# Performance work log

Measured on AMD Instinct MI355X. Metric: run time of the kernel, lower is better.

## Reference

```python
import jax, jax.numpy as jnp
import numpy as np
import math

L = 4      # model_layers
D = 512    # model_filters
H = 32     # heads = max(D//16, 1)
DH = D // H  # 16
S = 1024   # dataset_dimension == max_len == seq_len
B = 2
EPS = 1e-5


def setup_inputs() -> dict:
    key = jax.random.key(0)
    ks = jax.random.split(key, 12)
    scale = 0.02
    n = lambda k, shape: jax.random.normal(k, shape, dtype=jnp.float32) * scale
    return {
        "x": jax.random.normal(ks[0], (B, S), dtype=jnp.float32),
        "Winit": n(ks[1], (D,)),               # init_linear weight (1->D)
        "binit": jnp.zeros((D,), jnp.float32),
        "Wq": n(ks[2], (L, D, D)), "bq": jnp.zeros((L, D), jnp.float32),
        "Wk": n(ks[3], (L, D, D)), "bk": jnp.zeros((L, D), jnp.float32),
        "Wv": n(ks[4], (L, D, D)), "bv": jnp.zeros((L, D), jnp.float32),
        "Er": jax.random.normal(ks[5], (L, S, DH), dtype=jnp.float32) * scale,
        "Wlin": n(ks[6], (L, D, D)), "blin": jnp.zeros((L, D), jnp.float32),
        "ln_g": jnp.ones((L, D), jnp.float32), "ln_b": jnp.zeros((L, D), jnp.float32),
        "Wout": n(ks[7], (D, 1)),              # output_linear, no bias
    }


def layernorm(x, g, b):
    mu = jnp.mean(x, axis=-1, keepdims=True)
    var = jnp.mean(jnp.square(x - mu), axis=-1, keepdims=True)
    return (x - mu) * jax.lax.rsqrt(var + EPS) * g + b


def rel_attn(h, Wq, bq, Wk, bk, Wv, bv, Er):
    # h: [B, S, D]
    b_, s_, _ = h.shape
    q = (h @ Wq + bq).reshape(b_, s_, H, DH).transpose(0, 2, 1, 3)  # [B,H,S,dh]
    k = (h @ Wk + bk).reshape(b_, s_, H, DH).transpose(0, 2, 1, 3)
    v = (h @ Wv + bv).reshape(b_, s_, H, DH).transpose(0, 2, 1, 3)
    # relative-position term with skew trick (seq_len == max_len -> full Er)
    QEr = jnp.einsum('bhsd,td->bhst', q, Er)                  # [B,H,S,S]
    padded = jnp.pad(QEr, ((0, 0), (0, 0), (0, 0), (1, 0)))   # pad left of last dim
    Srel = padded.reshape(b_, H, s_ + 1, s_)[:, :, 1:, :]     # skew
    scores = (jnp.einsum('bhsd,bhtd->bhst', q, k) + Srel) / math.sqrt(DH)
    mask = jnp.tril(jnp.ones((s_, s_), dtype=bool))           # causal
    scores = jnp.where(mask, scores, -jnp.inf)
    p = jax.nn.softmax(scores, axis=-1)
    o = jnp.einsum('bhst,bhtd->bhsd', p, v)
    return o.transpose(0, 2, 1, 3).reshape(b_, s_, D)


def reference(x, Winit, binit, Wq, bq, Wk, bk, Wv, bv, Er, Wlin, blin, ln_g, ln_b, Wout):
    # init_linear(1->D) on scalar per position, then exact gelu
    h = jax.nn.gelu(x[..., None] * Winit + binit, approximate=False)  # [B,S,D]
    for l in range(L):
        a = rel_attn(h, Wq[l], bq[l], Wk[l], bk[l], Wv[l], bv[l], Er[l])
        y = layernorm(a @ Wlin[l] + blin[l], ln_g[l], ln_b[l])
        h = h + jax.nn.gelu(y, approximate=False)
    return h.sum(axis=-2) @ Wout  # [B,1]
```

## Files before the change

kernel.cpp:

```cpp
#include <hip/hip_runtime.h>
#include <math.h>

#define NL 4
#define DIM 512
#define NH 32
#define DHD 16
#define SEQ 1024
#define NB 2
#define LN_EPS 1e-5f
#define NEGF (-1e30f)
#define QSC 0.36067376022224085f

typedef _Float16 half4 __attribute__((ext_vector_type(4)));
typedef _Float16 half8 __attribute__((ext_vector_type(8)));
typedef float floatx4 __attribute__((ext_vector_type(4)));

__device__ __forceinline__ float gelu_exact(float x) {
    return 0.5f * x * (1.0f + erff(x * 0.70710678118654752f));
}

__device__ __forceinline__ void async16(const void* g, void* l) {
    __builtin_amdgcn_global_load_lds(
        (const __attribute__((address_space(1))) void*)g,
        (__attribute__((address_space(3))) void*)l, 16, 0, 0);
}

__global__ __launch_bounds__(256) void k_prep_all(const float* __restrict__ Wq,
        const float* __restrict__ Wk, const float* __restrict__ Wv,
        const float* __restrict__ Wlin, const float* __restrict__ bq,
        const float* __restrict__ bk, const float* __restrict__ bv,
        const float* __restrict__ Er, const float* __restrict__ x,
        const float* __restrict__ Wi, const float* __restrict__ bi,
        _Float16* __restrict__ Wqkvt, _Float16* __restrict__ Wlint,
        float* __restrict__ bqkv, _Float16* __restrict__ Erh,
        float* __restrict__ h, _Float16* __restrict__ hf) {
    __shared__ _Float16 lt[64][72];
    const int u = blockIdx.x;
    const int tid = threadIdx.x;
    if (u < 1024) {
        const int kx = u & 7, ny = (u >> 3) & 7, mz = u >> 6;
        const int l = mz >> 2, which = mz & 3;
        const float* src = (which == 0) ? Wq : (which == 1) ? Wk : (which == 2) ? Wv : Wlin;
        src += (size_t)l * 262144;
        const float scale = (which == 0) ? QSC : 1.0f;
        _Float16* dst = (which < 3) ? (Wqkvt + (size_t)l * 786432 + (size_t)which * 262144)
                                    : (Wlint + (size_t)l * 262144);
        const int k0 = kx << 6, n0 = ny << 6;
        #pragma unroll
        for (int p = 0; p < 4; p++) {
            int kl = (p << 4) + (tid >> 4);
            int n4 = (tid & 15) << 2;
            float4 wv = *(const float4*)(src + (size_t)(k0 + kl) * 512 + n0 + n4);
            lt[n4 + 0][kl] = (_Float16)(wv.x * scale);
            lt[n4 + 1][kl] = (_Float16)(wv.y * scale);
            lt[n4 + 2][kl] = (_Float16)(wv.z * scale);
            lt[n4 + 3][kl] = (_Float16)(wv.w * scale);
        }
        __syncthreads();
        int nl = tid >> 2, k16 = (tid & 3) << 4;
        float4* d4 = (float4*)(dst + (size_t)(n0 + nl) * 512 + k0 + k16);
        const float4* s4 = (const float4*)&lt[nl][k16];
        d4[0] = s4[0];
        d4[1] = s4[1];
    } else if (u < 2048) {
        int idx0 = ((u - 1024) << 10) + (tid << 2);
        int d = idx0 & 511, bs = idx0 >> 9;
        float xs = x[bs];
        float4 wv = *(const float4*)(Wi + d);
        float4 bv = *(const float4*)(bi + d);
        float4 r;
        r.x = gelu_exact(xs * wv.x + bv.x);
        r.y = gelu_exact(xs * wv.y + bv.y);
        r.z = gelu_exact(xs * wv.z + bv.z);
        r.w = gelu_exact(xs * wv.w + bv.w);
        *(float4*)(h + idx0) = r;
        half4 rh = {(_Float16)r.x, (_Float16)r.y, (_Float16)r.z, (_Float16)r.w};
        *(half4*)(hf + idx0) = rh;
    } else {
        int idx = ((u - 2048) << 8) + tid;
        if (idx < NL * 1536) {
            int l = idx / 1536, j = idx % 1536;
            int which = j >> 9, jj = j & 511;
            float val = (which == 0) ? bq[l * 512 + jj] * QSC
                      : (which == 1) ? bk[l * 512 + jj] : bv[l * 512 + jj];
            bqkv[idx] = val;
        }
        int e = idx - NL * 1536;
        if (e >= 0 && e < NL * SEQ * DHD) Erh[e] = (_Float16)Er[e];
    }
}

__global__ __launch_bounds__(256) void k_gemm_qkv(const _Float16* __restrict__ A,
        const _Float16* __restrict__ Bt, const float* __restrict__ bias,
        _Float16* __restrict__ o16) {
    __shared__ _Float16 As[2][128][32];
    __shared__ _Float16 Bs[2][96][32];
    const int tid = threadIdx.x;
    const int w = tid >> 6, lane = tid & 63;
    const int nn = lane & 15, qd = lane >> 4;
    const int wm = (w & 1) << 6;
    const int wn = (w >> 1) * 48;
    const int m0 = blockIdx.x << 7;
    const int n0 = blockIdx.y * 96;
    const int srow = lane >> 2, scol = (lane & 3) << 3;
    floatx4 acc[4][3] = {};
    for (int k0 = 0; k0 < 512; k0 += 64) {
        __syncthreads();
        #pragma unroll
        for (int p = 0; p < 2; p++) {
            #pragma unroll
            for (int hh = 0; hh < 2; hh++)
                async16(A + (size_t)(m0 + (hh << 6) + (w << 4) + srow) * 512
                          + k0 + (p << 5) + scol,
                        &As[p][(hh << 6) + (w << 4)][0]);
            async16(Bt + (size_t)(n0 + (w << 4) + srow) * 512 + k0 + (p << 5) + scol,
                    &Bs[p][(w << 4)][0]);
            if (w < 2)
                async16(Bt + (size_t)(n0 + 64 + (w << 4) + srow) * 512
                           + k0 + (p << 5) + scol,
                        &Bs[p][64 + (w << 4)][0]);
        }
        __syncthreads();
        #pragma unroll
        for (int ks = 0; ks < 2; ks++) {
            half8 af[4], bf[3];
            #pragma unroll
            for (int t = 0; t < 4; t++)
                af[t] = *(const half8*)&As[ks][wm + (t << 4) + nn][qd << 3];
            #pragma unroll
            for (int t = 0; t < 3; t++)
                bf[t] = *(const half8*)&Bs[ks][wn + (t << 4) + nn][qd << 3];
            #pragma unroll
            for (int ti = 0; ti < 4; ti++)
                #pragma unroll
                for (int tj = 0; tj < 3; tj++)
                    acc[ti][tj] = __builtin_amdgcn_mfma_f32_16x16x32_f16(
                            af[ti], bf[tj], acc[ti][tj], 0, 0, 0);
        }
    }
    float bv3[3];
    #pragma unroll
    for (int tj = 0; tj < 3; tj++) bv3[tj] = bias[n0 + wn + (tj << 4) + nn];
    #pragma unroll
    for (int ti = 0; ti < 4; ti++) {
        int rg = m0 + wm + (ti << 4) + (qd << 2);
        #pragma unroll
        for (int tj = 0; tj < 3; tj++) {
            int colg = n0 + wn + (tj << 4) + nn;
            int which = colg >> 9, ci = colg & 511;
            _Float16* op = o16 + (size_t)which * 1048576 + (size_t)rg * 512 + ci;
            #pragma unroll
            for (int r = 0; r < 4; r++)
                op[(size_t)r * 512] = (_Float16)(acc[ti][tj][r] + bv3[tj]);
        }
    }
}

__global__ __launch_bounds__(256) void k_gemm_lin(const _Float16* __restrict__ A,
        const _Float16* __restrict__ Bt, const float* __restrict__ bias,
        float* __restrict__ y) {
    __shared__ _Float16 As[2 * 64 * 32];
    __shared__ _Float16 Bs[2 * 64 * 32];
    const int tid = threadIdx.x;
    const int w = tid >> 6, lane = tid & 63;
    const int nn = lane & 15, qd = lane >> 4;
    const int wm = (w & 1) << 5, wn = (w >> 1) << 5;
    const int m0 = blockIdx.x << 6, n0 = blockIdx.y << 6;
    const int l2r = lane >> 2, l2c = (lane & 3) << 3;
    const _Float16* Ag = A + (size_t)(m0 + (w << 4) + l2r) * 512 + l2c;
    const _Float16* Bg = Bt + (size_t)(n0 + (w << 4) + l2r) * 512 + l2c;
    _Float16* Al = As + (w << 9);
    _Float16* Bl = Bs + (w << 9);
    floatx4 acc[2][2] = {};
    for (int k0 = 0; k0 < 512; k0 += 64) {
        __syncthreads();
        #pragma unroll
        for (int p = 0; p < 2; p++) {
            async16(Ag + k0 + (p << 5), Al + (p << 11));
            async16(Bg + k0 + (p << 5), Bl + (p << 11));
        }
        __syncthreads();
        #pragma unroll
        for (int ks = 0; ks < 2; ks++) {
            half8 af[2], bf[2];
            #pragma unroll
            for (int t = 0; t < 2; t++) {
                af[t] = *(const half8*)&As[(ks << 11) + ((wm + (t << 4) + nn) << 5) + (qd << 3)];
                bf[t] = *(const half8*)&Bs[(ks << 11) + ((wn + (t << 4) + nn) << 5) + (qd << 3)];
            }
            #pragma unroll
            for (int ti = 0; ti < 2; ti++)
                #pragma unroll
                for (int tj = 0; tj < 2; tj++)
                    acc[ti][tj] = __builtin_amdgcn_mfma_f32_16x16x32_f16(
                            af[ti], bf[tj], acc[ti][tj], 0, 0, 0);
        }
    }
    float bv2[2];
    #pragma unroll
    for (int tj = 0; tj < 2; tj++) bv2[tj] = bias[n0 + wn + (tj << 4) + nn];
    #pragma unroll
    for (int ti = 0; ti < 2; ti++) {
        int rg = m0 + wm + (ti << 4) + (qd << 2);
        #pragma unroll
        for (int tj = 0; tj < 2; tj++) {
            int colg = n0 + wn + (tj << 4) + nn;
            float* op = y + (size_t)rg * 512 + colg;
            #pragma unroll
            for (int r = 0; r < 4; r++)
                op[(size_t)r * 512] = acc[ti][tj][r] + bv2[tj];
        }
    }
}

__global__ __launch_bounds__(512) void k_attn_mfma(const _Float16* __restrict__ q,
        const _Float16* __restrict__ k, const _Float16* __restrict__ v,
        const _Float16* __restrict__ Er, _Float16* __restrict__ aout) {
    __shared__ _Float16 Ks[256][20];
    __shared__ _Float16 Vts[16][268];
    __shared__ float Rel[8][16][84];
    const int tid = threadIdx.x;
    const int w = tid >> 6, lane = tid & 63;
    const int wg = w & 3, half = w >> 2;
    const int nn = lane & 15, a4 = (lane >> 4) << 2;
    const int b_ = blockIdx.x >> 5, h_ = blockIdx.x & 31;
    const int y = blockIdx.y;
    const int r0p[2] = {64 * y, 64 * (15 - y)};
    const int R = r0p[1] + 64;

    half4 qf[2];
    floatx4 O[2];
    float m[2], lsum[2];
    #pragma unroll
    for (int ph = 0; ph < 2; ph++) {
        int s0w = r0p[ph] + (wg << 4);
        qf[ph] = *(const half4*)(q + ((size_t)(b_ * SEQ + s0w + nn)) * DIM + h_ * DHD + a4);
        O[ph] = (floatx4){0.f, 0.f, 0.f, 0.f};
        m[ph] = NEGF;
        lsum[ph] = 0.f;
    }

    for (int part = 0; part < 4; part++) {
        const int p0 = part << 8;
        if (p0 >= R) break;
        const int pend = (R < p0 + 256) ? R : (p0 + 256);
        __syncthreads();
        {
            int rl0 = tid >> 2, c4 = (tid & 3) << 2;
            for (int g = 0; g < pend - p0; g += 128) {
                int rl = g + rl0;
                if (rl < pend - p0) {
                    size_t gb = ((size_t)(b_ * SEQ + p0 + rl)) * DIM + h_ * DHD + c4;
                    *(half4*)&Ks[rl][c4] = *(const half4*)(k + gb);
                    half4 vv4 = *(const half4*)(v + gb);
                    Vts[c4 + 0][rl] = vv4.x;
                    Vts[c4 + 1][rl] = vv4.y;
                    Vts[c4 + 2][rl] = vv4.z;
                    Vts[c4 + 3][rl] = vv4.w;
                }
            }
        }
        __syncthreads();
        #pragma unroll
        for (int ph = 0; ph < 2; ph++) {
            const int r0 = r0p[ph];
            const int s0w = r0 + (wg << 4);
            const int hi = (r0 + 64 < pend) ? (r0 + 64) : pend;
            for (int ct = p0; ct < hi; ct += 64) {
                if (((ct >> 6) & 1) != half) continue;
                const int ctl = ct - p0;
                const int jbw = 1008 - s0w + ct;
                #pragma unroll
                for (int jt = 0; jt < 5; jt++) {
                    int j = jbw + (jt << 4) + nn;
                    j = (j < SEQ - 1) ? j : (SEQ - 1);
                    half4 ef = *(const half4*)(Er + (size_t)j * DHD + a4);
                    floatx4 racc = {0.f, 0.f, 0.f, 0.f};
                    racc = __builtin_amdgcn_mfma_f32_16x16x16f16(ef, qf[ph], racc, 0, 0, 0);
                    *(floatx4*)&Rel[w][nn][(jt << 4) + a4] = racc;
                }
                float st[4][4];
                const bool diag = (ct == r0);
                #pragma unroll
                for (int tt = 0; tt < 4; tt++) {
                    half4 kf = *(const half4*)&Ks[ctl + (tt << 4) + nn][a4];
                    floatx4 sacc = {0.f, 0.f, 0.f, 0.f};
                    sacc = __builtin_amdgcn_mfma_f32_16x16x16f16(kf, qf[ph], sacc, 0, 0, 0);
                    const float* rp = &Rel[w][nn][15 - nn + (tt << 4) + a4];
                    #pragma unroll
                    for (int r = 0; r < 4; r++) {
                        int tl = (tt << 4) + a4 + r;
                        float sv = sacc[r] + rp[r];
                        if (diag && (tl > (wg << 4) + nn)) sv = NEGF;
                        st[tt][r] = sv;
                    }
                }
                float cmax = NEGF;
                #pragma unroll
                for (int tt = 0; tt < 4; tt++)
                    #pragma unroll
                    for (int r = 0; r < 4; r++) cmax = fmaxf(cmax, st[tt][r]);
                cmax = fmaxf(cmax, __shfl_xor(cmax, 16));
                cmax = fmaxf(cmax, __shfl_xor(cmax, 32));
                float mnew = fmaxf(m[ph], cmax);
                float alpha = exp2f(m[ph] - mnew);
                m[ph] = mnew;
                float csum = 0.f;
                half4 pf[4];
                #pragma unroll
                for (int tt = 0; tt < 4; tt++) {
                    float p0e = exp2f(st[tt][0] - mnew);
                    float p1e = exp2f(st[tt][1] - mnew);
                    float p2e = exp2f(st[tt][2] - mnew);
                    float p3e = exp2f(st[tt][3] - mnew);
                    csum += (p0e + p1e) + (p2e + p3e);
                    half4 ph4 = {(_Float16)p0e, (_Float16)p1e, (_Float16)p2e, (_Float16)p3e};
                    pf[tt] = ph4;
                }
                lsum[ph] = lsum[ph] * alpha + csum;
                O[ph][0] *= alpha; O[ph][1] *= alpha; O[ph][2] *= alpha; O[ph][3] *= alpha;
                #pragma unroll
                for (int tt = 0; tt < 4; tt++) {
                    half4 vf = *(const half4*)&Vts[nn][ctl + (tt << 4) + a4];
                    O[ph] = __builtin_amdgcn_mfma_f32_16x16x16f16(vf, pf[tt], O[ph], 0, 0, 0);
                }
            }
        }
    }
    float* mb = (float*)Rel;
    __syncthreads();
    if (half == 1) {
        #pragma unroll
        for (int ph = 0; ph < 2; ph++) {
            int base = (((wg << 1) + ph) << 6) + lane;
            mb[base]        = O[ph][0];
            mb[base + 1024] = O[ph][1];
            mb[base + 2048] = O[ph][2];
            mb[base + 3072] = O[ph][3];
            mb[base + 4096] = m[ph];
            mb[base + 5120] = lsum[ph];
        }
    }
    __syncthreads();
    if (half == 0) {
        #pragma unroll
        for (int ph = 0; ph < 2; ph++) {
            int base = (((wg << 1) + ph) << 6) + lane;
            float m1 = mb[base + 4096];
            float l1 = mb[base + 5120];
            float mm = fmaxf(m[ph], m1);
            float a0 = exp2f(m[ph] - mm);
            float a1 = exp2f(m1 - mm);
            float lt = lsum[ph] * a0 + l1 * a1;
            lt += __shfl_xor(lt, 16);
            lt += __shfl_xor(lt, 32);
            float linv = 1.0f / lt;
            float o0 = (O[ph][0] * a0 + mb[base]        * a1) * linv;
            float o1 = (O[ph][1] * a0 + mb[base + 1024] * a1) * linv;
            float o2 = (O[ph][2] * a0 + mb[base + 2048] * a1) * linv;
            float o3 = (O[ph][3] * a0 + mb[base + 3072] * a1) * linv;
            int s0w = r0p[ph] + (wg << 4);
            half4 ov = {(_Float16)o0, (_Float16)o1, (_Float16)o2, (_Float16)o3};
            *(half4*)(aout + ((size_t)(b_ * SEQ + s0w + nn)) * DIM + h_ * DHD + a4) = ov;
        }
    }
}

__global__ __launch_bounds__(256) void k_ln_gelu_res(const float* __restrict__ y,
        const float* __restrict__ gam, const float* __restrict__ bet,
        float* __restrict__ h, _Float16* __restrict__ hf) {
    int row = (blockIdx.x << 2) + (threadIdx.x >> 6);
    int lane = threadIdx.x & 63;
    const float* yr = y + (size_t)row * DIM + (lane << 3);
    float4 v0 = *(const float4*)(yr);
    float4 v1 = *(const float4*)(yr + 4);
    float sum = (v0.x + v0.y) + (v0.z + v0.w) + (v1.x + v1.y) + (v1.z + v1.w);
    float sq = v0.x*v0.x + v0.y*v0.y + v0.z*v0.z + v0.w*v0.w
             + v1.x*v1.x + v1.y*v1.y + v1.z*v1.z + v1.w*v1.w;
    #pragma unroll
    for (int off = 32; off > 0; off >>= 1) {
        sum += __shfl_xor(sum, off);
        sq  += __shfl_xor(sq, off);
    }
    float mu = sum * (1.0f / DIM);
    float var = sq * (1.0f / DIM) - mu * mu;
    float rs = rsqrtf(var + LN_EPS);
    float4 g0 = *(const float4*)(gam + (lane << 3));
    float4 g1 = *(const float4*)(gam + (lane << 3) + 4);
    float4 b0 = *(const float4*)(bet + (lane << 3));
    float4 b1 = *(const float4*)(bet + (lane << 3) + 4);
    float* hr = h + (size_t)row * DIM + (lane << 3);
    float4 h0 = *(const float4*)(hr);
    float4 h1 = *(const float4*)(hr + 4);
    float o[8];
    o[0] = h0.x + gelu_exact((v0.x - mu) * rs * g0.x + b0.x);
    o[1] = h0.y + gelu_exact((v0.y - mu) * rs * g0.y + b0.y);
    o[2] = h0.z + gelu_exact((v0.z - mu) * rs * g0.z + b0.z);
    o[3] = h0.w + gelu_exact((v0.w - mu) * rs * g0.w + b0.w);
    o[4] = h1.x + gelu_exact((v1.x - mu) * rs * g1.x + b1.x);
    o[5] = h1.y + gelu_exact((v1.y - mu) * rs * g1.y + b1.y);
    o[6] = h1.z + gelu_exact((v1.z - mu) * rs * g1.z + b1.z);
    o[7] = h1.w + gelu_exact((v1.w - mu) * rs * g1.w + b1.w);
    *(float4*)(hr)     = make_float4(o[0], o[1], o[2], o[3]);
    *(float4*)(hr + 4) = make_float4(o[4], o[5], o[6], o[7]);
    half8 oh = {(_Float16)o[0], (_Float16)o[1], (_Float16)o[2], (_Float16)o[3],
                (_Float16)o[4], (_Float16)o[5], (_Float16)o[6], (_Float16)o[7]};
    *(half8*)(hf + (size_t)row * DIM + (lane << 3)) = oh;
}

__global__ __launch_bounds__(256) void k_colsum1(const float* __restrict__ h,
        float* __restrict__ pa) {
    int bt = blockIdx.x;
    int base = bt << 3;
    int tid = threadIdx.x;
    #pragma unroll
    for (int half = 0; half < 2; half++) {
        int d = (half << 8) + tid;
        float acc = 0.f;
        #pragma unroll
        for (int i = 0; i < 8; i++)
            acc += h[(size_t)(base + i) * DIM + d];
        pa[(size_t)bt * DIM + d] = acc;
    }
}

__global__ __launch_bounds__(256) void k_colsum2(const float* __restrict__ pa,
        float* __restrict__ pb) {
    __shared__ float red[4][64];
    int b = blockIdx.x, dt = blockIdx.y;
    int tid = threadIdx.x;
    int c = tid & 63, ig = tid >> 6;
    int d = (dt << 6) + c;
    float s = 0.f;
    for (int i = ig; i < 128; i += 4)
        s += pa[(size_t)(b * 128 + i) * DIM + d];
    red[ig][c] = s;
    __syncthreads();
    if (ig == 0)
        pb[(size_t)b * DIM + d] = red[0][c] + red[1][c] + red[2][c] + red[3][c];
}

__global__ __launch_bounds__(256) void k_final(const float* __restrict__ pb,
        const float* __restrict__ Wout, float* __restrict__ out) {
    __shared__ float red[4][2];
    int tid = threadIdx.x;
    float acc0 = 0.f, acc1 = 0.f;
    #pragma unroll
    for (int half = 0; half < 2; half++) {
        int d = (half << 8) + tid;
        float w = Wout[d];
        acc0 += pb[d] * w;
        acc1 += pb[DIM + d] * w;
    }
    #pragma unroll
    for (int off = 32; off > 0; off >>= 1) {
        acc0 += __shfl_down(acc0, off);
        acc1 += __shfl_down(acc1, off);
    }
    if ((tid & 63) == 0) { red[tid >> 6][0] = acc0; red[tid >> 6][1] = acc1; }
    __syncthreads();
    if (tid == 0) {
        out[0] = red[0][0] + red[1][0] + red[2][0] + red[3][0];
        out[1] = red[0][1] + red[1][1] + red[2][1] + red[3][1];
    }
}

extern "C" void kernel_launch(void* const* d_in, const int* in_sizes, int n_in,
                              void* d_out, int out_size, void* d_ws, size_t ws_size,
                              hipStream_t stream) {
    const float* x    = (const float*)d_in[0];
    const float* Wi   = (const float*)d_in[1];
    const float* bi   = (const float*)d_in[2];
    const float* Wq   = (const float*)d_in[3];
    const float* bq   = (const float*)d_in[4];
    const float* Wk   = (const float*)d_in[5];
    const float* bk   = (const float*)d_in[6];
    const float* Wv   = (const float*)d_in[7];
    const float* bv   = (const float*)d_in[8];
    const float* Er   = (const float*)d_in[9];
    const float* Wlin = (const float*)d_in[10];
    const float* blin = (const float*)d_in[11];
    const float* lng  = (const float*)d_in[12];
    const float* lnb  = (const float*)d_in[13];
    const float* Wout = (const float*)d_in[14];
    float* out = (float*)d_out;

    float* ws = (float*)d_ws;
    const size_t N1 = 1048576;
    float*     h     = ws;
    _Float16*  hf    = (_Float16*)(ws + N1);
    _Float16*  qh    = (_Float16*)(ws + N1 + N1/2);
    _Float16*  ah    = (_Float16*)(ws + 3 * N1);
    float*     y     = ws + 3 * N1 + N1/2;
    _Float16*  Wqkvt = (_Float16*)(ws + 4 * N1 + N1/2);
    _Float16*  Wlint = (_Float16*)(ws + 6 * N1);
    float*     bqkv  = ws + 6 * N1 + N1/2;
    _Float16*  Erh   = (_Float16*)(ws + 6 * N1 + N1/2 + 8192);
    float*     pa    = ws + 6 * N1 + N1/2 + 8192 + 32768;
    float*     pb    = pa + 131072;

    k_prep_all<<<dim3(2328), dim3(256), 0, stream>>>(Wq, Wk, Wv, Wlin, bq, bk, bv,
            Er, x, Wi, bi, Wqkvt, Wlint, bqkv, Erh, h, hf);
    for (int l = 0; l < NL; l++) {
        k_gemm_qkv<<<dim3(16, 16), dim3(256), 0, stream>>>(
                hf, Wqkvt + (size_t)l * 786432, bqkv + l * 1536, qh);
        k_attn_mfma<<<dim3(NB * NH, 8), dim3(512), 0, stream>>>(
                qh, qh + 1048576, qh + 2097152, Erh + (size_t)l * 16384, ah);
        k_gemm_lin<<<dim3(32, 8), dim3(256), 0, stream>>>(
                ah, Wlint + (size_t)l * 262144, blin + l * 512, y);
        k_ln_gelu_res<<<dim3(512), dim3(256), 0, stream>>>(
                y, lng + l * 512, lnb + l * 512, h, hf);
    }
    k_colsum1<<<dim3(256), dim3(256), 0, stream>>>(h, pa);
    k_colsum2<<<dim3(2, 8), dim3(256), 0, stream>>>(pa, pb);
    k_final<<<dim3(1), dim3(256), 0, stream>>>(pb, Wout, out);
}
```

Before: 300.8 us.

## Split attention key tiles across four wave groups with ring-buffered relative scores

Doubles the attention block to 1024 threads so four wave groups, instead of two, each take every fourth 64-key tile, and merges their partial softmax states in shared memory at the end. The relative-position scratch becomes a 32-column ring buffer per wave, and the QK MFMA is interleaved with the Er MFMA loop so each ring slot is consumed right after it is written. This aims to raise parallelism per block and cut LDS footprint, at the cost of a longer three-way merge and higher register pressure under the launch_bounds(1024, 8) hint.

```diff
diff --git a/kernel.cpp b/kernel.cpp
--- a/kernel.cpp
+++ b/kernel.cpp
@@ -213,15 +213,15 @@
     }
 }
 
-__global__ __launch_bounds__(512) void k_attn_mfma(const _Float16* __restrict__ q,
+__global__ __launch_bounds__(1024, 8) void k_attn_mfma(const _Float16* __restrict__ q,
         const _Float16* __restrict__ k, const _Float16* __restrict__ v,
         const _Float16* __restrict__ Er, _Float16* __restrict__ aout) {
     __shared__ _Float16 Ks[256][20];
     __shared__ _Float16 Vts[16][268];
-    __shared__ float Rel[8][16][84];
+    __shared__ float Ring[16][16][36];
     const int tid = threadIdx.x;
     const int w = tid >> 6, lane = tid & 63;
-    const int wg = w & 3, half = w >> 2;
+    const int wg = w & 3, quar = w >> 2;
     const int nn = lane & 15, a4 = (lane >> 4) << 2;
     const int b_ = blockIdx.x >> 5, h_ = blockIdx.x & 31;
     const int y = blockIdx.y;
@@ -246,18 +246,15 @@
         const int pend = (R < p0 + 256) ? R : (p0 + 256);
         __syncthreads();
         {
-            int rl0 = tid >> 2, c4 = (tid & 3) << 2;
-            for (int g = 0; g < pend - p0; g += 128) {
-                int rl = g + rl0;
-                if (rl < pend - p0) {
-                    size_t gb = ((size_t)(b_ * SEQ + p0 + rl)) * DIM + h_ * DHD + c4;
-                    *(half4*)&Ks[rl][c4] = *(const half4*)(k + gb);
-                    half4 vv4 = *(const half4*)(v + gb);
-                    Vts[c4 + 0][rl] = vv4.x;
-                    Vts[c4 + 1][rl] = vv4.y;
-                    Vts[c4 + 2][rl] = vv4.z;
-                    Vts[c4 + 3][rl] = vv4.w;
-                }
+            int rl = tid >> 2, c4 = (tid & 3) << 2;
+            if (rl < pend - p0) {
+                size_t gb = ((size_t)(b_ * SEQ + p0 + rl)) * DIM + h_ * DHD + c4;
+                *(half4*)&Ks[rl][c4] = *(const half4*)(k + gb);
+                half4 vv4 = *(const half4*)(v + gb);
+                Vts[c4 + 0][rl] = vv4.x;
+                Vts[c4 + 1][rl] = vv4.y;
+                Vts[c4 + 2][rl] = vv4.z;
+                Vts[c4 + 3][rl] = vv4.w;
             }
         }
         __syncthreads();
@@ -267,9 +264,12 @@
             const int s0w = r0 + (wg << 4);
             const int hi = (r0 + 64 < pend) ? (r0 + 64) : pend;
             for (int ct = p0; ct < hi; ct += 64) {
-                if (((ct >> 6) & 1) != half) continue;
+                if (((ct >> 6) & 3) != quar) continue;
                 const int ctl = ct - p0;
                 const int jbw = 1008 - s0w + ct;
+                const bool diag = (ct == r0);
+                const int xb = 15 - nn + a4;
+                float st[4][4];
                 #pragma unroll
                 for (int jt = 0; jt < 5; jt++) {
                     int j = jbw + (jt << 4) + nn;
@@ -277,22 +277,19 @@
                     half4 ef = *(const half4*)(Er + (size_t)j * DHD + a4);
                     floatx4 racc = {0.f, 0.f, 0.f, 0.f};
                     racc = __builtin_amdgcn_mfma_f32_16x16x16f16(ef, qf[ph], racc, 0, 0, 0);
-                    *(floatx4*)&Rel[w][nn][(jt << 4) + a4] = racc;
-                }
-                float st[4][4];
-                const bool diag = (ct == r0);
-                #pragma unroll
-                for (int tt = 0; tt < 4; tt++) {
-                    half4 kf = *(const half4*)&Ks[ctl + (tt << 4) + nn][a4];
-                    floatx4 sacc = {0.f, 0.f, 0.f, 0.f};
-                    sacc = __builtin_amdgcn_mfma_f32_16x16x16f16(kf, qf[ph], sacc, 0, 0, 0);
-                    const float* rp = &Rel[w][nn][15 - nn + (tt << 4) + a4];
-                    #pragma unroll
-                    for (int r = 0; r < 4; r++) {
-                        int tl = (tt << 4) + a4 + r;
-                        float sv = sacc[r] + rp[r];
-                        if (diag && (tl > (wg << 4) + nn)) sv = NEGF;
-                        st[tt][r] = sv;
+                    *(floatx4*)&Ring[w][nn][((jt << 4) & 31) + a4] = racc;
+                    if (jt >= 1) {
+                        const int tt = jt - 1;
+                        half4 kf = *(const half4*)&Ks[ctl + (tt << 4) + nn][a4];
+                        floatx4 sacc = {0.f, 0.f, 0.f, 0.f};
+                        sacc = __builtin_amdgcn_mfma_f32_16x16x16f16(kf, qf[ph], sacc, 0, 0, 0);
+                        #pragma unroll
+                        for (int r = 0; r < 4; r++) {
+                            int tl = (tt << 4) + a4 + r;
+                            float sv = sacc[r] + Ring[w][nn][((tt << 4) + xb + r) & 31];
+                            if (diag && (tl > (wg << 4) + nn)) sv = NEGF;
+                            st[tt][r] = sv;
+                        }
                     }
                 }
                 float cmax = NEGF;
@@ -327,40 +324,47 @@
             }
         }
     }
-    float* mb = (float*)Rel;
+    float* mb = (float*)Ring;
     __syncthreads();
-    if (half == 1) {
+    if (quar != 0) {
         #pragma unroll
         for (int ph = 0; ph < 2; ph++) {
-            int base = (((wg << 1) + ph) << 6) + lane;
-            mb[base]        = O[ph][0];
-            mb[base + 1024] = O[ph][1];
-            mb[base + 2048] = O[ph][2];
-            mb[base + 3072] = O[ph][3];
-            mb[base + 4096] = m[ph];
-            mb[base + 5120] = lsum[ph];
+            int st = (((quar - 1) << 3) + (wg << 1) + ph) * 384 + lane;
+            mb[st]       = O[ph][0];
+            mb[st + 64]  = O[ph][1];
+            mb[st + 128] = O[ph][2];
+            mb[st + 192] = O[ph][3];
+            mb[st + 256] = m[ph];
+            mb[st + 320] = lsum[ph];
         }
     }
     __syncthreads();
-    if (half == 0) {
+    if (quar == 0) {
         #pragma unroll
         for (int ph = 0; ph < 2; ph++) {
-            int base = (((wg << 1) + ph) << 6) + lane;
-            float m1 = mb[base + 4096];
-            float l1 = mb[base + 5120];
-            float mm = fmaxf(m[ph], m1);
-            float a0 = exp2f(m[ph] - mm);
-            float a1 = exp2f(m1 - mm);
-            float lt = lsum[ph] * a0 + l1 * a1;
-            lt += __shfl_xor(lt, 16);
-            lt += __shfl_xor(lt, 32);
-            float linv = 1.0f / lt;
-            float o0 = (O[ph][0] * a0 + mb[base]        * a1) * linv;
-            float o1 = (O[ph][1] * a0 + mb[base + 1024] * a1) * linv;
-            float o2 = (O[ph][2] * a0 + mb[base + 2048] * a1) * linv;
-            float o3 = (O[ph][3] * a0 + mb[base + 3072] * a1) * linv;
+            float mm = m[ph], ll = lsum[ph];
+            floatx4 Oo = O[ph];
+            #pragma unroll
+            for (int qq = 1; qq < 4; qq++) {
+                int st = (((qq - 1) << 3) + (wg << 1) + ph) * 384 + lane;
+                float mq = mb[st + 256];
+                float lq = mb[st + 320];
+                float nm = fmaxf(mm, mq);
+                float a0 = exp2f(mm - nm);
+                float a1 = exp2f(mq - nm);
+                Oo[0] = Oo[0] * a0 + mb[st]       * a1;
+                Oo[1] = Oo[1] * a0 + mb[st + 64]  * a1;
+                Oo[2] = Oo[2] * a0 + mb[st + 128] * a1;
+                Oo[3] = Oo[3] * a0 + mb[st + 192] * a1;
+                ll = ll * a0 + lq * a1;
+                mm = nm;
+            }
+            ll += __shfl_xor(ll, 16);
+            ll += __shfl_xor(ll, 32);
+            float linv = 1.0f / ll;
             int s0w = r0p[ph] + (wg << 4);
-            half4 ov = {(_Float16)o0, (_Float16)o1, (_Float16)o2, (_Float16)o3};
+            half4 ov = { (_Float16)(Oo[0] * linv), (_Float16)(Oo[1] * linv),
+                         (_Float16)(Oo[2] * linv), (_Float16)(Oo[3] * linv) };
             *(half4*)(aout + ((size_t)(b_ * SEQ + s0w + nn)) * DIM + h_ * DHD + a4) = ov;
         }
     }
@@ -504,7 +508,7 @@
     for (int l = 0; l < NL; l++) {
         k_gemm_qkv<<<dim3(16, 16), dim3(256), 0, stream>>>(
                 hf, Wqkvt + (size_t)l * 786432, bqkv + l * 1536, qh);
-        k_attn_mfma<<<dim3(NB * NH, 8), dim3(512), 0, stream>>>(
+        k_attn_mfma<<<dim3(NB * NH, 8), dim3(1024), 0, stream>>>(
                 qh, qh + 1048576, qh + 2097152, Erh + (size_t)l * 16384, ah);
         k_gemm_lin<<<dim3(32, 8), dim3(256), 0, stream>>>(
                 ah, Wlint + (size_t)l * 262144, blin + l * 512, y);
```

New measurement: 326.6 us. 8.6% more time.
